# Kernel tuning notes

Hardware: AMD Instinct MI355X
Metric: run time of the kernel (lower is better)

The kernel has to match this reference:

```python
import jax, jax.numpy as jnp
import numpy as np

HEADS = 16

def setup_inputs() -> dict:
    key = jax.random.key(0)
    ks = jax.random.split(key, 5)
    dim = 1024
    x = jax.random.normal(ks[0], (2, 2048, dim), dtype=jnp.float32)
    scale = 1.0 / np.sqrt(dim)
    Wq = jax.random.normal(ks[1], (dim, dim), dtype=jnp.float32) * scale
    Wk = jax.random.normal(ks[2], (dim, dim), dtype=jnp.float32) * scale
    Wv = jax.random.normal(ks[3], (dim, dim), dtype=jnp.float32) * scale
    Wo = jax.random.normal(ks[4], (dim, dim), dtype=jnp.float32) * scale
    return {"x": x, "Wq": Wq, "Wk": Wk, "Wv": Wv, "Wo": Wo}

def reference(x, Wq, Wk, Wv, Wo):
    b, n, dim = x.shape
    h = HEADS
    d = dim // h
    # projections: torch Linear y = x @ W.T (W is [out,in])
    def split_heads(t):
        return t.reshape(b, n, h, d).transpose(0, 2, 1, 3)  # b h n d
    q = split_heads(x @ Wq.T)
    k = split_heads(x @ Wk.T)
    v = split_heads(x @ Wv.T)
    scale = jnp.asarray(d, x.dtype) ** -0.5
    dots = jnp.einsum('bhid,bhjd->bhij', q, k) * scale
    # causal mask: positions j > i masked (triu with diagonal 1 since i == j)
    i_idx = jnp.arange(n)[:, None]
    j_idx = jnp.arange(n)[None, :]
    mask_value = -jnp.finfo(dots.dtype).max
    dots = jnp.where(j_idx > i_idx, mask_value, dots)
    attn = jax.nn.softmax(dots, axis=-1)  # dropout p=0 (eval) is identity
    out = jnp.einsum('bhij,bhjd->bhid', attn, v)
    out = out.transpose(0, 2, 1, 3).reshape(b, n, dim)
    return out @ Wo.T
```

## Files before the change

### kernel.cpp

```cpp
#include <hip/hip_runtime.h>
#include <hip/hip_bf16.h>

#define BATCH 2
#define SEQ   2048
#define DIM   1024
#define HEADS 16
#define DIMH  64
#define BK    32
#define LOG2E 1.44269504088896340736f
#define SM_SHIFT 16.0f

typedef __attribute__((ext_vector_type(8))) short short8;
typedef __attribute__((ext_vector_type(4))) short short4v;
typedef __attribute__((ext_vector_type(4))) float floatx4;

static __device__ __forceinline__ void gload_lds16(const void* g, void* l) {
    __builtin_amdgcn_global_load_lds(
        (const __attribute__((address_space(1))) void*)g,
        (__attribute__((address_space(3))) void*)l, 16, 0, 0);
}

static __device__ __forceinline__ unsigned pkbf(float a, float b) {
    __hip_bfloat16 ta = __float2bfloat16(a);
    __hip_bfloat16 tb = __float2bfloat16(b);
    return (unsigned)*reinterpret_cast<unsigned short*>(&ta) |
           ((unsigned)*reinterpret_cast<unsigned short*>(&tb) << 16);
}

__global__ __launch_bounds__(256) void conv_bf16(
    const float* __restrict__ x,  const float* __restrict__ Wq,
    const float* __restrict__ Wk, const float* __restrict__ Wv,
    __hip_bfloat16* __restrict__ dst)
{
    const size_t NX = (size_t)BATCH * SEQ * DIM;
    const size_t NW = (size_t)DIM * DIM;
    size_t i = ((size_t)blockIdx.x * 256 + threadIdx.x) * 4;
    if (i >= NX + 3 * NW) return;
    const float* src; size_t off;
    if (i < NX) { src = x; off = i; }
    else {
        size_t j = i - NX;
        int w = (int)(j >> 20);
        src = (w == 0) ? Wq : (w == 1) ? Wk : Wv;
        off = j & (NW - 1);
    }
    floatx4 f = *reinterpret_cast<const floatx4*>(src + off);
    short4v o;
    #pragma unroll
    for (int e = 0; e < 4; ++e) {
        __hip_bfloat16 t = __float2bfloat16(f[e]);
        o[e] = *reinterpret_cast<short*>(&t);
    }
    *reinterpret_cast<short4v*>((short*)dst + i) = o;
}

__global__ __launch_bounds__(256) void conv_wo(
    const float* __restrict__ W, __hip_bfloat16* __restrict__ dst)
{
    size_t i = ((size_t)blockIdx.x * 256 + threadIdx.x) * 4;
    floatx4 f = *reinterpret_cast<const floatx4*>(W + i);
    short4v o;
    #pragma unroll
    for (int e = 0; e < 4; ++e) {
        __hip_bfloat16 t = __float2bfloat16(f[e]);
        o[e] = *reinterpret_cast<short*>(&t);
    }
    *reinterpret_cast<short4v*>((short*)dst + i) = o;
}

__global__ __launch_bounds__(256) void gemm_qkv(
    const __hip_bfloat16* __restrict__ xbf,
    const __hip_bfloat16* __restrict__ wbf,
    __hip_bfloat16* __restrict__ qkv)
{
    __shared__ __align__(16) short As[128 * BK];
    __shared__ __align__(16) short Bs[128 * BK];

    const int tid  = threadIdx.x;
    const int wv   = tid >> 6;
    const int lane = tid & 63;
    const int quad = lane >> 4;
    const int l16  = lane & 15;
    const int wm   = wv >> 1, wn = wv & 1;
    const int m0   = blockIdx.x * 128;
    const int n0   = blockIdx.y * 128;
    const int z    = n0 >> 10;
    __hip_bfloat16* out = qkv + (size_t)z * (BATCH * SEQ * DIM);

    const int srow = tid >> 2;
    const int scol = (tid & 3) * 8;

    floatx4 acc[4][4] = {};

    for (int k0 = 0; k0 < DIM; k0 += BK) {
        __syncthreads();
        #pragma unroll
        for (int i = 0; i < 2; ++i) {
            const __hip_bfloat16* ga = xbf + (size_t)(m0 + srow + i * 64) * DIM + k0 + scol;
            const __hip_bfloat16* gb = wbf + (size_t)(n0 + srow + i * 64) * DIM + k0 + scol;
            gload_lds16(ga, (char*)As + i * 4096 + wv * 1024);
            gload_lds16(gb, (char*)Bs + i * 4096 + wv * 1024);
        }
        __syncthreads();

        short8 af[4], bf[4];
        #pragma unroll
        for (int mt = 0; mt < 4; ++mt)
            af[mt] = *reinterpret_cast<const short8*>(&As[(wm * 64 + mt * 16 + l16) * 32 + quad * 8]);
        #pragma unroll
        for (int nt = 0; nt < 4; ++nt)
            bf[nt] = *reinterpret_cast<const short8*>(&Bs[(wn * 64 + nt * 16 + l16) * 32 + quad * 8]);
        #pragma unroll
        for (int mt = 0; mt < 4; ++mt)
            #pragma unroll
            for (int nt = 0; nt < 4; ++nt)
                acc[mt][nt] = __builtin_amdgcn_mfma_f32_16x16x32_bf16(
                    af[mt], bf[nt], acc[mt][nt], 0, 0, 0);
    }

    const float esc = (z == 0) ? (0.125f * LOG2E) : 1.0f;
    #pragma unroll
    for (int mt = 0; mt < 4; ++mt) {
        #pragma unroll
        for (int nt = 0; nt < 4; ++nt) {
            const int n  = n0 + wn * 64 + nt * 16 + l16;
            const int hh = (n >> 6) & 15, dv = n & 63;
            #pragma unroll
            for (int r = 0; r < 4; ++r) {
                const int m  = m0 + wm * 64 + mt * 16 + quad * 4 + r;
                const int bb = m >> 11, nn = m & (SEQ - 1);
                const float v = acc[mt][nt][r] * esc;
                if (z < 2)
                    out[((size_t)(bb * HEADS + hh) * SEQ + nn) * DIMH + dv] = __float2bfloat16(v);
                else
                    out[((size_t)(bb * HEADS + hh) * DIMH + dv) * SEQ + nn] = __float2bfloat16(v);
            }
        }
    }
}

__global__ __launch_bounds__(256) void gemm_out(
    const __hip_bfloat16* __restrict__ A,
    const __hip_bfloat16* __restrict__ W,
    float* __restrict__ C)
{
    __shared__ __align__(16) short As[128 * BK];
    __shared__ __align__(16) short Bs[128 * BK];

    const int tid  = threadIdx.x;
    const int wv   = tid >> 6;
    const int lane = tid & 63;
    const int quad = lane >> 4;
    const int l16  = lane & 15;
    const int wm   = wv >> 1, wn = wv & 1;
    const int m0   = blockIdx.x * 128;
    const int n0   = blockIdx.y * 128;

    const int srow = tid >> 2;
    const int scol = (tid & 3) * 8;

    floatx4 acc[4][4] = {};

    for (int k0 = 0; k0 < DIM; k0 += BK) {
        __syncthreads();
        #pragma unroll
        for (int i = 0; i < 2; ++i) {
            const __hip_bfloat16* ga = A + (size_t)(m0 + srow + i * 64) * DIM + k0 + scol;
            const __hip_bfloat16* gb = W + (size_t)(n0 + srow + i * 64) * DIM + k0 + scol;
            gload_lds16(ga, (char*)As + i * 4096 + wv * 1024);
            gload_lds16(gb, (char*)Bs + i * 4096 + wv * 1024);
        }
        __syncthreads();

        short8 af[4], bf[4];
        #pragma unroll
        for (int mt = 0; mt < 4; ++mt)
            af[mt] = *reinterpret_cast<const short8*>(&As[(wm * 64 + mt * 16 + l16) * 32 + quad * 8]);
        #pragma unroll
        for (int nt = 0; nt < 4; ++nt)
            bf[nt] = *reinterpret_cast<const short8*>(&Bs[(wn * 64 + nt * 16 + l16) * 32 + quad * 8]);
        #pragma unroll
        for (int mt = 0; mt < 4; ++mt)
            #pragma unroll
            for (int nt = 0; nt < 4; ++nt)
                acc[mt][nt] = __builtin_amdgcn_mfma_f32_16x16x32_bf16(
                    af[mt], bf[nt], acc[mt][nt], 0, 0, 0);
    }

    #pragma unroll
    for (int mt = 0; mt < 4; ++mt)
        #pragma unroll
        for (int nt = 0; nt < 4; ++nt) {
            const int n = n0 + wn * 64 + nt * 16 + l16;
            #pragma unroll
            for (int r = 0; r < 4; ++r) {
                const int m = m0 + wm * 64 + mt * 16 + quad * 4 + r;
                C[(size_t)m * DIM + n] = acc[mt][nt][r];
            }
        }
}

__global__ __launch_bounds__(128) void attn_causal(
    const __hip_bfloat16* __restrict__ qkv,
    __hip_bfloat16* __restrict__ omat)
{
    __shared__ __align__(16) short kt[64 * 64];
    __shared__ __align__(16) short vt[64 * 64];
    __shared__ __align__(16) short pt[2][16 * 72];

    const int id    = blockIdx.x;
    const int combo = id & 31;
    const int p     = id >> 5;
    const int b     = combo >> 4;
    const int h     = combo & 15;
    const int tA = p, tB = 63 - p;
    const int nA = (tA + 2) >> 1;
    const int nB = (tB + 2) >> 1;
    const int total = nA + nB;

    const size_t hoff = (size_t)(b * HEADS + h) * SEQ * DIMH;
    const size_t one  = (size_t)BATCH * SEQ * DIM;
    const __hip_bfloat16* qb  = qkv + hoff;
    const __hip_bfloat16* kb  = qkv + one + hoff;
    const __hip_bfloat16* vtg = qkv + 2 * one + hoff;

    const int tid  = threadIdx.x;
    const int wv   = tid >> 6;
    const int lane = tid & 63;
    const int quad = lane >> 4;
    const int l16  = lane & 15;
    const int xr   = l16 & 7;

    const short8 kones = {0x3F80, 0x3F80, 0x3F80, 0x3F80,
                          0x3F80, 0x3F80, 0x3F80, 0x3F80};

    int q16 = tA * 32 + wv * 16;
    short8 aq0 = *reinterpret_cast<const short8*>(qb + (size_t)(q16 + l16) * DIMH + quad * 8);
    short8 aq1 = *reinterpret_cast<const short8*>(qb + (size_t)(q16 + l16) * DIMH + 32 + quad * 8);
    floatx4 oacc[4] = {};
    floatx4 lsum = {};

    short8 kreg[4], vreg[4];
    #pragma unroll
    for (int i = 0; i < 4; ++i) {
        const int c = tid + 128 * i;
        const int row = c >> 3, jc = c & 7;
        kreg[i] = *reinterpret_cast<const short8*>(kb + (size_t)row * DIMH + jc * 8);
        vreg[i] = *reinterpret_cast<const short8*>(vtg + (size_t)row * SEQ + jc * 8);
    }

    for (int s = 0; s < total; ++s) {
        const bool lastA = (s == nA - 1);
        const int j0 = ((s < nA) ? s : s - nA) * 64;

        __syncthreads();
        #pragma unroll
        for (int i = 0; i < 4; ++i) {
            const int c = tid + 128 * i;
            const int row = c >> 3, jc = c & 7;
            const int off = row * 64 + ((jc ^ (row & 7)) * 8);
            *reinterpret_cast<short8*>(&kt[off]) = kreg[i];
            *reinterpret_cast<short8*>(&vt[off]) = vreg[i];
        }
        __syncthreads();

        if (s + 1 < total) {
            const int s2 = s + 1;
            const int j1 = ((s2 < nA) ? s2 : s2 - nA) * 64;
            #pragma unroll
            for (int i = 0; i < 4; ++i) {
                const int c = tid + 128 * i;
                const int row = c >> 3, jc = c & 7;
                kreg[i] = *reinterpret_cast<const short8*>(kb + (size_t)(j1 + row) * DIMH + jc * 8);
                vreg[i] = *reinterpret_cast<const short8*>(vtg + (size_t)row * SEQ + j1 + jc * 8);
            }
        }

        floatx4 st[4];
        #pragma unroll
        for (int t = 0; t < 4; ++t) {
            const int rw = t * 16 + l16;
            short8 a0 = *reinterpret_cast<const short8*>(&kt[rw * 64 + (quad ^ xr) * 8]);
            short8 a1 = *reinterpret_cast<const short8*>(&kt[rw * 64 + ((quad + 4) ^ xr) * 8]);
            floatx4 zz = {};
            zz    = __builtin_amdgcn_mfma_f32_16x16x32_bf16(a0, aq0, zz, 0, 0, 0);
            st[t] = __builtin_amdgcn_mfma_f32_16x16x32_bf16(a1, aq1, zz, 0, 0, 0);
        }

        if (j0 + 63 > q16) {
            const int qg = q16 + l16;
            #pragma unroll
            for (int t = 0; t < 4; ++t)
                #pragma unroll
                for (int r = 0; r < 4; ++r) {
                    const int jg = j0 + t * 16 + quad * 4 + r;
                    if (jg > qg) st[t][r] = -3.0e38f;
                }
        }

        #pragma unroll
        for (int t = 0; t < 4; ++t)
            #pragma unroll
            for (int r = 0; r < 4; ++r)
                st[t][r] = __builtin_amdgcn_exp2f(st[t][r] - SM_SHIFT);

        #pragma unroll
        for (int t = 0; t < 4; ++t) {
            *reinterpret_cast<unsigned*>(&pt[wv][l16 * 72 + t * 16 + quad * 4]) =
                pkbf(st[t][0], st[t][1]);
            *reinterpret_cast<unsigned*>(&pt[wv][l16 * 72 + t * 16 + quad * 4 + 2]) =
                pkbf(st[t][2], st[t][3]);
        }
        short8 p0 = *reinterpret_cast<const short8*>(&pt[wv][l16 * 72 + quad * 8]);
        short8 p1 = *reinterpret_cast<const short8*>(&pt[wv][l16 * 72 + 32 + quad * 8]);

        lsum = __builtin_amdgcn_mfma_f32_16x16x32_bf16(kones, p0, lsum, 0, 0, 0);
        lsum = __builtin_amdgcn_mfma_f32_16x16x32_bf16(kones, p1, lsum, 0, 0, 0);

        #pragma unroll
        for (int dt = 0; dt < 4; ++dt) {
            const int rw = dt * 16 + l16;
            short8 v0 = *reinterpret_cast<const short8*>(&vt[rw * 64 + (quad ^ xr) * 8]);
            short8 v1 = *reinterpret_cast<const short8*>(&vt[rw * 64 + ((quad + 4) ^ xr) * 8]);
            oacc[dt] = __builtin_amdgcn_mfma_f32_16x16x32_bf16(v0, p0, oacc[dt], 0, 0, 0);
            oacc[dt] = __builtin_amdgcn_mfma_f32_16x16x32_bf16(v1, p1, oacc[dt], 0, 0, 0);
        }

        if (lastA || s == total - 1) {
            const float rl = 1.0f / lsum[0];
            #pragma unroll
            for (int dt = 0; dt < 4; ++dt)
                #pragma unroll
                for (int r = 0; r < 4; ++r) {
                    const int dv = dt * 16 + quad * 4 + r;
                    omat[(size_t)(b * SEQ + q16 + l16) * DIM + h * DIMH + dv] =
                        __float2bfloat16(oacc[dt][r] * rl);
                }
            if (lastA) {
                q16 = tB * 32 + wv * 16;
                aq0 = *reinterpret_cast<const short8*>(qb + (size_t)(q16 + l16) * DIMH + quad * 8);
                aq1 = *reinterpret_cast<const short8*>(qb + (size_t)(q16 + l16) * DIMH + 32 + quad * 8);
                #pragma unroll
                for (int dt = 0; dt < 4; ++dt)
                    #pragma unroll
                    for (int r = 0; r < 4; ++r) oacc[dt][r] = 0.f;
                #pragma unroll
                for (int r = 0; r < 4; ++r) lsum[r] = 0.f;
            }
        }
    }
}


extern "C" void kernel_launch(void* const* d_in, const int* in_sizes, int n_in,
                              void* d_out, int out_size, void* d_ws, size_t ws_size,
                              hipStream_t stream) {
    const float* x  = (const float*)d_in[0];
    const float* Wq = (const float*)d_in[1];
    const float* Wk = (const float*)d_in[2];
    const float* Wv = (const float*)d_in[3];
    const float* Wo = (const float*)d_in[4];

    __hip_bfloat16* qkv  = (__hip_bfloat16*)d_ws;
    __hip_bfloat16* omat = qkv + (size_t)3 * BATCH * SEQ * DIM;
    __hip_bfloat16* wobf = (__hip_bfloat16*)d_ws;

    __hip_bfloat16* xbf = (__hip_bfloat16*)d_out;
    __hip_bfloat16* wbf = xbf + (size_t)BATCH * SEQ * DIM;

    conv_bf16 <<<7168, 256, 0, stream>>>(x, Wq, Wk, Wv, xbf);
    gemm_qkv  <<<dim3((BATCH * SEQ) / 128, (3 * DIM) / 128), 256, 0, stream>>>(xbf, wbf, qkv);
    attn_causal<<<dim3(1024), 128, 0, stream>>>(qkv, omat);
    conv_wo   <<<1024, 256, 0, stream>>>(Wo, wobf);
    gemm_out  <<<dim3((BATCH * SEQ) / 128, DIM / 128),       256, 0, stream>>>(omat, wobf, (float*)d_out);
}
```

Measured before the change: 194.6 us.

## Merge Wo conversion into input cast and write attention output in head layout

Folds the Wo bf16 conversion into the single input-conversion kernel, which removes one launch. The attention kernel now writes its output in place over Q in per-head [b,h,n,d] layout with contiguous 64-element rows, instead of scattering into a separate [b,n,dim] matrix. The output GEMM reads A through head-strided addressing to match. It also swaps round-to-nearest bf16 packing of the softmax probabilities for plain truncation, which is cheaper but slightly less accurate.

```diff
diff --git a/kernel.cpp b/kernel.cpp
--- a/kernel.cpp
+++ b/kernel.cpp
@@ -20,52 +20,39 @@
         (__attribute__((address_space(3))) void*)l, 16, 0, 0);
 }
 
-static __device__ __forceinline__ unsigned pkbf(float a, float b) {
-    __hip_bfloat16 ta = __float2bfloat16(a);
-    __hip_bfloat16 tb = __float2bfloat16(b);
-    return (unsigned)*reinterpret_cast<unsigned short*>(&ta) |
-           ((unsigned)*reinterpret_cast<unsigned short*>(&tb) << 16);
-}
-
-__global__ __launch_bounds__(256) void conv_bf16(
+static __device__ __forceinline__ unsigned pk_trunc(float a, float b) {
+    return (__float_as_uint(b) & 0xffff0000u) | (__float_as_uint(a) >> 16);
+}
+
+__global__ __launch_bounds__(256) void conv_all(
     const float* __restrict__ x,  const float* __restrict__ Wq,
     const float* __restrict__ Wk, const float* __restrict__ Wv,
-    __hip_bfloat16* __restrict__ dst)
+    const float* __restrict__ Wo,
+    __hip_bfloat16* __restrict__ dst, __hip_bfloat16* __restrict__ dwo)
 {
     const size_t NX = (size_t)BATCH * SEQ * DIM;
     const size_t NW = (size_t)DIM * DIM;
     size_t i = ((size_t)blockIdx.x * 256 + threadIdx.x) * 4;
-    if (i >= NX + 3 * NW) return;
-    const float* src; size_t off;
-    if (i < NX) { src = x; off = i; }
-    else {
+    if (i >= NX + 4 * NW) return;
+    const float* src; __hip_bfloat16* d;
+    if (i < NX) { src = x + i; d = dst + i; }
+    else if (i < NX + 3 * NW) {
         size_t j = i - NX;
         int w = (int)(j >> 20);
-        src = (w == 0) ? Wq : (w == 1) ? Wk : Wv;
-        off = j & (NW - 1);
-    }
-    floatx4 f = *reinterpret_cast<const floatx4*>(src + off);
+        src = ((w == 0) ? Wq : (w == 1) ? Wk : Wv) + (j & (NW - 1));
+        d = dst + i;
+    } else {
+        size_t off = i - (NX + 3 * NW);
+        src = Wo + off; d = dwo + off;
+    }
+    floatx4 f = *reinterpret_cast<const floatx4*>(src);
     short4v o;
     #pragma unroll
     for (int e = 0; e < 4; ++e) {
         __hip_bfloat16 t = __float2bfloat16(f[e]);
         o[e] = *reinterpret_cast<short*>(&t);
     }
-    *reinterpret_cast<short4v*>((short*)dst + i) = o;
-}
-
-__global__ __launch_bounds__(256) void conv_wo(
-    const float* __restrict__ W, __hip_bfloat16* __restrict__ dst)
-{
-    size_t i = ((size_t)blockIdx.x * 256 + threadIdx.x) * 4;
-    floatx4 f = *reinterpret_cast<const floatx4*>(W + i);
-    short4v o;
-    #pragma unroll
-    for (int e = 0; e < 4; ++e) {
-        __hip_bfloat16 t = __float2bfloat16(f[e]);
-        o[e] = *reinterpret_cast<short*>(&t);
-    }
-    *reinterpret_cast<short4v*>((short*)dst + i) = o;
+    *reinterpret_cast<short4v*>(d) = o;
 }
 
 __global__ __launch_bounds__(256) void gemm_qkv(
@@ -140,7 +127,7 @@
 }
 
 __global__ __launch_bounds__(256) void gemm_out(
-    const __hip_bfloat16* __restrict__ A,
+    const __hip_bfloat16* __restrict__ qhs,
     const __hip_bfloat16* __restrict__ W,
     float* __restrict__ C)
 {
@@ -162,13 +149,17 @@
     floatx4 acc[4][4] = {};
 
     for (int k0 = 0; k0 < DIM; k0 += BK) {
+        const int h    = k0 >> 6;
+        const int koff = k0 & 63;
         __syncthreads();
         #pragma unroll
         for (int i = 0; i < 2; ++i) {
-            const __hip_bfloat16* ga = A + (size_t)(m0 + srow + i * 64) * DIM + k0 + scol;
-            const __hip_bfloat16* gb = W + (size_t)(n0 + srow + i * 64) * DIM + k0 + scol;
-            gload_lds16(ga, (char*)As + i * 4096 + wv * 1024);
-            gload_lds16(gb, (char*)Bs + i * 4096 + wv * 1024);
+            const int m  = m0 + srow + i * 64;
+            const int bb = m >> 11, nn = m & (SEQ - 1);
+            gload_lds16(qhs + ((size_t)(bb * HEADS + h) * SEQ + nn) * DIMH + koff + scol,
+                        (char*)As + i * 4096 + wv * 1024);
+            gload_lds16(W + (size_t)(n0 + srow + i * 64) * DIM + k0 + scol,
+                        (char*)Bs + i * 4096 + wv * 1024);
         }
         __syncthreads();
 
@@ -201,8 +192,7 @@
 }
 
 __global__ __launch_bounds__(128) void attn_causal(
-    const __hip_bfloat16* __restrict__ qkv,
-    __hip_bfloat16* __restrict__ omat)
+    __hip_bfloat16* __restrict__ qkv)
 {
     __shared__ __align__(16) short kt[64 * 64];
     __shared__ __align__(16) short vt[64 * 64];
@@ -220,7 +210,7 @@
 
     const size_t hoff = (size_t)(b * HEADS + h) * SEQ * DIMH;
     const size_t one  = (size_t)BATCH * SEQ * DIM;
-    const __hip_bfloat16* qb  = qkv + hoff;
+    __hip_bfloat16* qb        = qkv + hoff;
     const __hip_bfloat16* kb  = qkv + one + hoff;
     const __hip_bfloat16* vtg = qkv + 2 * one + hoff;
 
@@ -231,7 +221,7 @@
     const int l16  = lane & 15;
     const int xr   = l16 & 7;
 
-    const short8 kones = {0x3F80, 0x3F80, 0x3F80, 0x3F80,
+    const short8 kone8 = {0x3F80, 0x3F80, 0x3F80, 0x3F80,
                           0x3F80, 0x3F80, 0x3F80, 0x3F80};
 
     int q16 = tA * 32 + wv * 16;
@@ -307,15 +297,15 @@
         #pragma unroll
         for (int t = 0; t < 4; ++t) {
             *reinterpret_cast<unsigned*>(&pt[wv][l16 * 72 + t * 16 + quad * 4]) =
-                pkbf(st[t][0], st[t][1]);
+                pk_trunc(st[t][0], st[t][1]);
             *reinterpret_cast<unsigned*>(&pt[wv][l16 * 72 + t * 16 + quad * 4 + 2]) =
-                pkbf(st[t][2], st[t][3]);
+                pk_trunc(st[t][2], st[t][3]);
         }
         short8 p0 = *reinterpret_cast<const short8*>(&pt[wv][l16 * 72 + quad * 8]);
         short8 p1 = *reinterpret_cast<const short8*>(&pt[wv][l16 * 72 + 32 + quad * 8]);
 
-        lsum = __builtin_amdgcn_mfma_f32_16x16x32_bf16(kones, p0, lsum, 0, 0, 0);
-        lsum = __builtin_amdgcn_mfma_f32_16x16x32_bf16(kones, p1, lsum, 0, 0, 0);
+        lsum = __builtin_amdgcn_mfma_f32_16x16x32_bf16(kone8, p0, lsum, 0, 0, 0);
+        lsum = __builtin_amdgcn_mfma_f32_16x16x32_bf16(kone8, p1, lsum, 0, 0, 0);
 
         #pragma unroll
         for (int dt = 0; dt < 4; ++dt) {
@@ -331,11 +321,9 @@
             #pragma unroll
             for (int dt = 0; dt < 4; ++dt)
                 #pragma unroll
-                for (int r = 0; r < 4; ++r) {
-                    const int dv = dt * 16 + quad * 4 + r;
-                    omat[(size_t)(b * SEQ + q16 + l16) * DIM + h * DIMH + dv] =
+                for (int r = 0; r < 4; ++r)
+                    qb[(size_t)(q16 + l16) * DIMH + dt * 16 + quad * 4 + r] =
                         __float2bfloat16(oacc[dt][r] * rl);
-                }
             if (lastA) {
                 q16 = tB * 32 + wv * 16;
                 aq0 = *reinterpret_cast<const short8*>(qb + (size_t)(q16 + l16) * DIMH + quad * 8);
@@ -362,15 +350,13 @@
     const float* Wo = (const float*)d_in[4];
 
     __hip_bfloat16* qkv  = (__hip_bfloat16*)d_ws;
-    __hip_bfloat16* omat = qkv + (size_t)3 * BATCH * SEQ * DIM;
-    __hip_bfloat16* wobf = (__hip_bfloat16*)d_ws;
+    __hip_bfloat16* wobf = (__hip_bfloat16*)((char*)d_ws + (size_t)24 * 1024 * 1024);
 
     __hip_bfloat16* xbf = (__hip_bfloat16*)d_out;
     __hip_bfloat16* wbf = xbf + (size_t)BATCH * SEQ * DIM;
 
-    conv_bf16 <<<7168, 256, 0, stream>>>(x, Wq, Wk, Wv, xbf);
+    conv_all  <<<8192, 256, 0, stream>>>(x, Wq, Wk, Wv, Wo, xbf, wobf);
     gemm_qkv  <<<dim3((BATCH * SEQ) / 128, (3 * DIM) / 128), 256, 0, stream>>>(xbf, wbf, qkv);
-    attn_causal<<<dim3(1024), 128, 0, stream>>>(qkv, omat);
-    conv_wo   <<<1024, 256, 0, stream>>>(Wo, wobf);
-    gemm_out  <<<dim3((BATCH * SEQ) / 128, DIM / 128),       256, 0, stream>>>(omat, wobf, (float*)d_out);
-}
+    attn_causal<<<dim3(1024), 128, 0, stream>>>(qkv);
+    gemm_out  <<<dim3((BATCH * SEQ) / 128, DIM / 128), 256, 0, stream>>>(qkv, wobf, (float*)d_out);
+}
```

New measurement: 192.0 us. About the same (-1.4%).
